# Kernel optimization log

Measured on AMD Instinct MI355X. Metric: run time of the kernel, lower is better.

## Reference

```python
import jax, jax.numpy as jnp
import numpy as np

N, E = 50000, 800000
F_IN, HID, HEADS = 128, 32, 8
H1 = HID * HEADS            # 256: conv1 concat output, also conv2 in/out
NUM_WALKS, WALK_LEN = 512, 64
WINDOW, NEG_S = 5, 10
TEMP = 0.07
NEG_SLOPE = 0.2


def setup_inputs() -> dict:
    key = jax.random.key(0)
    ks = jax.random.split(key, 16)
    inp = {
        "x": jax.random.normal(ks[0], (N, F_IN), jnp.float32),
        "edge_index": jax.random.randint(ks[1], (2, E), 0, N),
        "walks": jax.random.randint(ks[2], (NUM_WALKS, WALK_LEN), 0, N),
        "neg_nodes": jax.random.randint(ks[3], (NUM_WALKS, WALK_LEN, NEG_S), 0, N),
        # conv1 params (GATConv: in=F_IN, out=HID, heads=HEADS, concat)
        "W1": jax.random.normal(ks[4], (F_IN, HEADS * HID), jnp.float32) / np.sqrt(F_IN),
        "a_src1": jax.random.normal(ks[5], (HEADS, HID), jnp.float32) / np.sqrt(HID),
        "a_dst1": jax.random.normal(ks[6], (HEADS, HID), jnp.float32) / np.sqrt(HID),
        "b1": jnp.zeros((HEADS * HID,), jnp.float32),
        # conv2 params (GATConv: in=H1, out=H1, heads=1)
        "W2": jax.random.normal(ks[7], (H1, H1), jnp.float32) / np.sqrt(H1),
        "a_src2": jax.random.normal(ks[8], (1, H1), jnp.float32) / np.sqrt(H1),
        "a_dst2": jax.random.normal(ks[9], (1, H1), jnp.float32) / np.sqrt(H1),
        "b2": jnp.zeros((H1,), jnp.float32),
    }
    return inp


def gat_conv(x, edge_index, W, a_src, a_dst, b, heads, out_ch):
    """PyG-style GATConv: self-loops, per-dst softmax attention, concat heads."""
    n = x.shape[0]
    loops = jnp.arange(n)
    src = jnp.concatenate([edge_index[0], loops])
    dst = jnp.concatenate([edge_index[1], loops])
    xw = (x @ W).reshape(n, heads, out_ch)                  # [N,H,C]
    al_s = jnp.einsum('nhc,hc->nh', xw, a_src)              # [N,H]
    al_d = jnp.einsum('nhc,hc->nh', xw, a_dst)
    e = jax.nn.leaky_relu(al_s[src] + al_d[dst], NEG_SLOPE)  # [Et,H]
    m = jax.ops.segment_max(e, dst, num_segments=n)
    ex = jnp.exp(e - m[dst])
    den = jax.ops.segment_sum(ex, dst, num_segments=n)
    alpha = ex / den[dst]                                    # [Et,H]
    out = jax.ops.segment_sum(alpha[:, :, None] * xw[src], dst, num_segments=n)
    return out.reshape(n, heads * out_ch) + b


def walk_contrastive_loss(emb, walks, neg_nodes):
    eps = 1e-8
    nrm = emb / jnp.clip(jnp.linalg.norm(emb, axis=-1, keepdims=True), eps)
    L = walks.shape[1]
    offs = jnp.concatenate([jnp.arange(-WINDOW, 0), jnp.arange(1, WINDOW + 1)])  # [2W]
    pos_pos = jnp.arange(L)[:, None] + offs[None, :]        # [L,2W]
    pos_valid = (pos_pos >= 0) & (pos_pos < L)
    pos_nodes = walks[:, jnp.clip(pos_pos, 0, L - 1)]       # [B,L,2W]
    anchor = nrm[walks]                                      # [B,L,D]
    pos_sims = jnp.einsum('bld,blpd->blp', anchor, nrm[pos_nodes]) / TEMP
    neg_sims = jnp.einsum('bld,blsd->bls', anchor, nrm[neg_nodes]) / TEMP
    # drop negatives that collide with (valid) positives, as torch.isin filter does
    neg_in_pos = ((neg_nodes[:, :, :, None] == pos_nodes[:, :, None, :])
                  & pos_valid[None, :, None, :]).any(-1)     # [B,L,S]
    pos_sum = jnp.sum(jnp.exp(pos_sims) * pos_valid[None].astype(emb.dtype), axis=-1)
    neg_sum = jnp.sum(jnp.exp(neg_sims) * (~neg_in_pos).astype(emb.dtype), axis=-1)
    has_pos = pos_valid.any(-1)[None]                        # [1,L]
    safe_pos = jnp.where(has_pos, pos_sum, 1.0)
    term = -jnp.log(safe_pos / (safe_pos + neg_sum))
    return jnp.sum(jnp.where(has_pos, term, 0.0))


def reference(x, edge_index, walks, neg_nodes, W1, a_src1, a_dst1, b1,
              W2, a_src2, a_dst2, b2):
    emb1 = jax.nn.elu(gat_conv(x, edge_index, W1, a_src1, a_dst1, b1, HEADS, HID))
    emb2 = gat_conv(emb1, edge_index, W2, a_src2, a_dst2, b2, 1, H1)
    emb = jnp.concatenate([emb1, emb2], axis=1)              # [N, 2*H1]
    return walk_contrastive_loss(emb, walks, neg_nodes)
```

## Files before the change

### kernel.cpp

```cpp
#include <hip/hip_runtime.h>
#include <math.h>

#define N_NODES 50000
#define N_PAD 50048
#define E_EDGES 800000
#define E_PAD (E_EDGES + 8 * N_NODES)
#define FDIM_IN 128
#define HID_1 32
#define HEADS_1 8
#define H1DIM 256
#define NUM_WALKS 512
#define WALK_LEN 64
#define WINDOW 5
#define NEG_S 10
#define TEMP 0.07f
#define INV_TEMP (1.0f / 0.07f)
#define NEG_SLOPE 0.2f
#define LOG2E 1.44269504f

#define SCAN_BLOCKS ((N_NODES + 255) / 256)

typedef unsigned int uint;
typedef unsigned short ushort;
typedef long long i64_t;
typedef __attribute__((ext_vector_type(8))) short bf16x8;
typedef __attribute__((ext_vector_type(8))) ushort us8;
typedef __attribute__((ext_vector_type(4))) float f32x4;
typedef __attribute__((ext_vector_type(2))) float vf2;

__device__ __forceinline__ float leaky(float v) {
    return fmaxf(v, v * NEG_SLOPE);
}

__device__ __forceinline__ float bfl(uint u) { return __uint_as_float(u << 16); }
__device__ __forceinline__ float bfh(uint u) { return __uint_as_float(u & 0xffff0000u); }

__device__ __forceinline__ ushort f2bf(float x) {
    uint u = __float_as_uint(x);
    u = u + 0x7fffu + ((u >> 16) & 1u);
    return (ushort)(u >> 16);
}

__device__ __forceinline__ uint pk4fp8(float a, float b, float c, float d) {
    int u = __builtin_amdgcn_cvt_pk_fp8_f32(a, b, 0, false);
    u = __builtin_amdgcn_cvt_pk_fp8_f32(c, d, u, true);
    return (uint)u;
}


#define PB_CVT  6250
#define PB_DEG  3125
#define PB_FILL ((E_PAD / 2 + 255) / 256)
#define PO_DEG  (PB_CVT)
#define PO_FILL (PO_DEG + PB_DEG)
#define PO_WT1  (PO_FILL + PB_FILL)
#define PO_WT2  (PO_WT1 + 128)
#define PO_MISC (PO_WT2 + 256)
#define PREP_GRID (PO_MISC + 1)

__global__ __launch_bounds__(256) void prep_kernel(
        const float* __restrict__ x, const int* __restrict__ ei,
        const float* __restrict__ W1, const float* __restrict__ W2,
        uint* __restrict__ xb, ushort* __restrict__ wt1, ushort* __restrict__ wt2,
        int* __restrict__ deg, uint* __restrict__ srl_u,
        float* __restrict__ als1, float* __restrict__ als2, uint* __restrict__ xw8) {
    const int blk = blockIdx.x, t = threadIdx.x;
    if (blk < PB_CVT) {
        int i = blk * 256 + t;
        float4 v = ((const float4*)x)[i];
        uint2 p;
        p.x = (uint)f2bf(v.x) | ((uint)f2bf(v.y) << 16);
        p.y = (uint)f2bf(v.z) | ((uint)f2bf(v.w) << 16);
        ((uint2*)xb)[i] = p;
    } else if (blk < PO_FILL) {
        int e = (blk - PO_DEG) * 256 + t;
        atomicAdd(&deg[ei[E_EDGES + e]], 1);
    } else if (blk < PO_WT1) {
        int i = (blk - PO_FILL) * 256 + t;
        if (i < E_PAD / 2) srl_u[i] = 0xC350C350u;
    } else if (blk < PO_WT2) {
        int tid = (blk - PO_WT1) * 256 + t;
        int k = tid >> 8, n = tid & 255;
        wt1[n * 128 + k] = f2bf(W1[k * 256 + n]);
    } else if (blk < PO_MISC) {
        int tid = (blk - PO_WT2) * 256 + t;
        int k = tid >> 8, n = tid & 255;
        wt2[n * 256 + k] = f2bf(W2[k * 256 + n]);
    } else {
        if (t < HEADS_1) als1[N_NODES * HEADS_1 + t] = -1e30f;
        if (t == HEADS_1) als2[N_NODES] = -1e30f;
        if (t >= 64 && t < 128) xw8[N_NODES * 64 + (t - 64)] = 0u;
    }
}


__global__ __launch_bounds__(256) void scan_a(const int* __restrict__ deg,
                                              int* __restrict__ excl,
                                              int* __restrict__ bsum) {
    __shared__ int s[256];
    int t = threadIdx.x;
    int i = blockIdx.x * 256 + t;
    int d = (i < N_NODES) ? deg[i] : 0;
    int v = (d + 7) & ~7;
    s[t] = v;
    __syncthreads();
    for (int off = 1; off < 256; off <<= 1) {
        int tmp = (t >= off) ? s[t - off] : 0;
        __syncthreads();
        s[t] += tmp;
        __syncthreads();
    }
    if (i < N_NODES) excl[i] = s[t] - v;
    if (t == 255) bsum[blockIdx.x] = s[255];
}

__global__ __launch_bounds__(256) void scan_b(int* __restrict__ bsum) {
    __shared__ int s[256];
    int t = threadIdx.x;
    int v = (t < SCAN_BLOCKS) ? bsum[t] : 0;
    s[t] = v;
    __syncthreads();
    for (int off = 1; off < 256; off <<= 1) {
        int tmp = (t >= off) ? s[t - off] : 0;
        __syncthreads();
        s[t] += tmp;
        __syncthreads();
    }
    if (t < SCAN_BLOCKS) bsum[t] = s[t] - v;
}

__global__ void scan_c2(const int* __restrict__ deg,
                        int* __restrict__ excl, const int* __restrict__ bsum,
                        int* __restrict__ row_start) {
    int i = blockIdx.x * blockDim.x + threadIdx.x;
    if (i < N_NODES) {
        int rs = excl[i] + bsum[i >> 8];
        row_start[i] = rs;
        if (i == N_NODES - 1) row_start[N_NODES] = rs + ((deg[i] + 7) & ~7);
    }
}

__global__ void bucket_kernel(const int* __restrict__ ei,
                              const int* __restrict__ row_start,
                              int* __restrict__ cursor,
                              ushort* __restrict__ srclist) {
    int e = blockIdx.x * blockDim.x + threadIdx.x;
    if (e >= E_EDGES) return;
    int dst = ei[E_EDGES + e];
    int pos = atomicAdd(&cursor[dst], 1);
    srclist[row_start[dst] + pos] = (ushort)ei[e];
}

template<int K, int H>
__global__ __launch_bounds__(256) void mfma_gemm64(
        const ushort* __restrict__ A,
        const ushort* __restrict__ Wt,
        uint* __restrict__ Y8,
        const float* __restrict__ a_src,
        const float* __restrict__ a_dst,
        float* __restrict__ als, float* __restrict__ ald) {
    constexpr int KP = K + 8;
    constexpr int K8 = K / 8;
    __shared__ __align__(16) ushort As[64 * KP];
    __shared__ float sals[64][5], sald[64][5];
    const int m0 = blockIdx.x * 64;
    const int t = threadIdx.x;
    const uint4* Ag = (const uint4*)(A + (size_t)m0 * K);
    uint4* As4 = (uint4*)As;
    for (int i = t; i < 64 * K8; i += 256) {
        int r = i / K8, c8 = i % K8;
        As4[r * (K8 + 1) + c8] = Ag[i];
    }
    __syncthreads();
    const int wv = __builtin_amdgcn_readfirstlane(t >> 6);
    const int lane = t & 63;
    const int n0 = wv * 64;
    const int mrow = lane & 15, q = lane >> 4;
    f32x4 acc[4][4];
#pragma unroll
    for (int mt = 0; mt < 4; mt++)
#pragma unroll
        for (int i = 0; i < 4; i++) acc[mt][i] = (f32x4){0.f, 0.f, 0.f, 0.f};
#pragma unroll
    for (int k0 = 0; k0 < K; k0 += 32) {
        bf16x8 a[4], b[4];
#pragma unroll
        for (int mt = 0; mt < 4; mt++)
            a[mt] = *(const bf16x8*)(As + (mt * 16 + mrow) * KP + k0 + q * 8);
#pragma unroll
        for (int i = 0; i < 4; i++)
            b[i] = *(const bf16x8*)(Wt + (uint)(n0 + i * 16 + mrow) * K + k0 + q * 8);
#pragma unroll
        for (int mt = 0; mt < 4; mt++)
#pragma unroll
            for (int i = 0; i < 4; i++)
                acc[mt][i] = __builtin_amdgcn_mfma_f32_16x16x32_bf16(a[mt], b[i], acc[mt][i], 0, 0, 0);
    }
    {
        float as[4], ad[4];
#pragma unroll
        for (int i = 0; i < 4; i++) {
            as[i] = a_src[n0 + i * 16 + mrow];
            ad[i] = a_dst[n0 + i * 16 + mrow];
        }
#pragma unroll
        for (int mt = 0; mt < 4; mt++) {
#pragma unroll
            for (int r = 0; r < 4; r++) {
                const int row = m0 + mt * 16 + q * 4 + r;
                if (H == 8) {
                    float ps0 = acc[mt][0][r] * as[0] + acc[mt][1][r] * as[1];
                    float ps1 = acc[mt][2][r] * as[2] + acc[mt][3][r] * as[3];
                    float pd0 = acc[mt][0][r] * ad[0] + acc[mt][1][r] * ad[1];
                    float pd1 = acc[mt][2][r] * ad[2] + acc[mt][3][r] * ad[3];
#pragma unroll
                    for (int o = 1; o < 16; o <<= 1) {
                        ps0 += __shfl_xor(ps0, o, 64); ps1 += __shfl_xor(ps1, o, 64);
                        pd0 += __shfl_xor(pd0, o, 64); pd1 += __shfl_xor(pd1, o, 64);
                    }
                    if (mrow == 0 && row < N_NODES) {
                        als[row * 8 + 2 * wv] = ps0 * LOG2E;
                        als[row * 8 + 2 * wv + 1] = ps1 * LOG2E;
                        ald[row * 8 + 2 * wv] = pd0 * LOG2E;
                        ald[row * 8 + 2 * wv + 1] = pd1 * LOG2E;
                    }
                } else {
                    float ps = acc[mt][0][r] * as[0] + acc[mt][1][r] * as[1]
                             + acc[mt][2][r] * as[2] + acc[mt][3][r] * as[3];
                    float pd = acc[mt][0][r] * ad[0] + acc[mt][1][r] * ad[1]
                             + acc[mt][2][r] * ad[2] + acc[mt][3][r] * ad[3];
#pragma unroll
                    for (int o = 1; o < 16; o <<= 1) {
                        ps += __shfl_xor(ps, o, 64); pd += __shfl_xor(pd, o, 64);
                    }
                    if (mrow == 0) {
                        sals[mt * 16 + q * 4 + r][wv] = ps;
                        sald[mt * 16 + q * 4 + r][wv] = pd;
                    }
                }
            }
        }
    }
    __syncthreads();
    if (H == 1 && t < 64) {
        const int row = m0 + t;
        if (row < N_NODES) {
            als[row] = (sals[t][0] + sals[t][1] + sals[t][2] + sals[t][3]) * LOG2E;
            ald[row] = (sald[t][0] + sald[t][1] + sald[t][2] + sald[t][3]) * LOG2E;
        }
    }
    float* S = (float*)As + wv * 16 * 68;
    const int prow = lane >> 2, pj = lane & 3;
#pragma unroll
    for (int mt = 0; mt < 4; mt++) {
#pragma unroll
        for (int i = 0; i < 4; i++)
#pragma unroll
            for (int r = 0; r < 4; r++)
                S[(q * 4 + r) * 68 + i * 16 + mrow] = acc[mt][i][r];
        const float* cp = S + prow * 68 + pj * 16;
        uint4 o;
        o.x = pk4fp8(cp[0],  cp[1],  cp[2],  cp[3]);
        o.y = pk4fp8(cp[4],  cp[5],  cp[6],  cp[7]);
        o.z = pk4fp8(cp[8],  cp[9],  cp[10], cp[11]);
        o.w = pk4fp8(cp[12], cp[13], cp[14], cp[15]);
        const int row = m0 + mt * 16 + prow;
        if (row < N_NODES)
            ((uint4*)(Y8 + (size_t)row * 64))[wv * 4 + pj] = o;
    }
}

__global__ __launch_bounds__(256) void gat_gather1(
        const int* __restrict__ row_start, const ushort* __restrict__ srclist,
        const float* __restrict__ als, const float* __restrict__ ald,
        const uint* __restrict__ xw8,
        const float* __restrict__ bias,
        ushort* __restrict__ emb1b) {
    const int wid = __builtin_amdgcn_readfirstlane(blockIdx.x * 4 + (threadIdx.x >> 6));
    const uint lane = threadIdx.x & 63;
    const uint h = lane >> 3;
    const float ald_n = ald[wid * HEADS_1 + h];
    const int beg = row_start[wid], end = row_start[wid + 1];

    float ex0 = __builtin_amdgcn_exp2f(leaky(als[wid * HEADS_1 + h] + ald_n));
    uint u = xw8[((uint)wid << 6) + lane];
    vf2 lo = __builtin_amdgcn_cvt_pk_f32_fp8((int)u, false);
    vf2 hi = __builtin_amdgcn_cvt_pk_f32_fp8((int)u, true);
    float den = ex0;
    vf2 exv0 = {ex0, ex0};
    vf2 a01 = exv0 * lo, a23 = exv0 * hi;

    for (int i = beg; i < end; i += 8) {
        us8 sv = *(const us8*)(srclist + i);
        uint rr[8]; float ee[8];
#pragma unroll
        for (int j = 0; j < 8; j++) rr[j] = xw8[((uint)sv[j] << 6) + lane];
#pragma unroll
        for (int j = 0; j < 8; j++) ee[j] = als[(uint)sv[j] * HEADS_1 + h];
#pragma unroll
        for (int j = 0; j < 8; j++) {
            float ex = __builtin_amdgcn_exp2f(leaky(ee[j] + ald_n));
            vf2 l2 = __builtin_amdgcn_cvt_pk_f32_fp8((int)rr[j], false);
            vf2 h2 = __builtin_amdgcn_cvt_pk_f32_fp8((int)rr[j], true);
            den += ex;
            vf2 exv = {ex, ex};
            a01 += exv * l2;
            a23 += exv * h2;
        }
    }
    float inv = 1.f / den;
    float4 bv = ((const float4*)bias)[lane];
    float4 r;
    r.x = a01[0] * inv + bv.x; r.y = a01[1] * inv + bv.y;
    r.z = a23[0] * inv + bv.z; r.w = a23[1] * inv + bv.w;
    r.x = r.x > 0.f ? r.x : __expf(r.x) - 1.f;
    r.y = r.y > 0.f ? r.y : __expf(r.y) - 1.f;
    r.z = r.z > 0.f ? r.z : __expf(r.z) - 1.f;
    r.w = r.w > 0.f ? r.w : __expf(r.w) - 1.f;
    uint2 p;
    p.x = (uint)f2bf(r.x) | ((uint)f2bf(r.y) << 16);
    p.y = (uint)f2bf(r.z) | ((uint)f2bf(r.w) << 16);
    ((uint2*)emb1b)[((uint)wid << 6) + lane] = p;
}

__global__ __launch_bounds__(256) void gat_gather2(
        const int* __restrict__ row_start, const ushort* __restrict__ srclist,
        const float* __restrict__ als, const float* __restrict__ ald,
        const uint* __restrict__ xw8,
        const float* __restrict__ bias,
        const ushort* __restrict__ emb1b,
        uint* __restrict__ embn8) {
    const int wid = __builtin_amdgcn_readfirstlane(blockIdx.x * 4 + (threadIdx.x >> 6));
    const uint lane = threadIdx.x & 63;
    const float ald_n = ald[wid];
    const int beg = row_start[wid], end = row_start[wid + 1];

    float ex0 = __builtin_amdgcn_exp2f(leaky(als[wid] + ald_n));
    uint u = xw8[((uint)wid << 6) + lane];
    vf2 lo = __builtin_amdgcn_cvt_pk_f32_fp8((int)u, false);
    vf2 hi = __builtin_amdgcn_cvt_pk_f32_fp8((int)u, true);
    float den = ex0;
    vf2 exv0 = {ex0, ex0};
    vf2 a01 = exv0 * lo, a23 = exv0 * hi;

    for (int i = beg; i < end; i += 8) {
        us8 sv = *(const us8*)(srclist + i);
        uint rr[8]; float ee[8];
#pragma unroll
        for (int j = 0; j < 8; j++) rr[j] = xw8[((uint)sv[j] << 6) + lane];
#pragma unroll
        for (int j = 0; j < 8; j++) ee[j] = als[(uint)sv[j]];
#pragma unroll
        for (int j = 0; j < 8; j++) {
            float ex = __builtin_amdgcn_exp2f(leaky(ee[j] + ald_n));
            vf2 l2 = __builtin_amdgcn_cvt_pk_f32_fp8((int)rr[j], false);
            vf2 h2 = __builtin_amdgcn_cvt_pk_f32_fp8((int)rr[j], true);
            den += ex;
            vf2 exv = {ex, ex};
            a01 += exv * l2;
            a23 += exv * h2;
        }
    }
    float inv = 1.f / den;
    float4 bv = ((const float4*)bias)[lane];
    float4 e2;
    e2.x = a01[0] * inv + bv.x; e2.y = a01[1] * inv + bv.y;
    e2.z = a23[0] * inv + bv.z; e2.w = a23[1] * inv + bv.w;
    uint2 u1 = ((const uint2*)emb1b)[((uint)wid << 6) + lane];
    float4 e1;
    e1.x = bfl(u1.x); e1.y = bfh(u1.x); e1.z = bfl(u1.y); e1.w = bfh(u1.y);

    float ssum = e1.x * e1.x + e1.y * e1.y + e1.z * e1.z + e1.w * e1.w
               + e2.x * e2.x + e2.y * e2.y + e2.z * e2.z + e2.w * e2.w;
#pragma unroll
    for (int o = 32; o > 0; o >>= 1) ssum += __shfl_xor(ssum, o, 64);
    float innv = 1.f / fmaxf(sqrtf(ssum), 1e-8f);

    uint p1 = pk4fp8(e1.x * innv, e1.y * innv, e1.z * innv, e1.w * innv);
    uint p2 = pk4fp8(e2.x * innv, e2.y * innv, e2.z * innv, e2.w * innv);
    embn8[((uint)wid << 7) + lane] = p1;
    embn8[((uint)wid << 7) + 64 + lane] = p2;
}


#define ROWU 130

__global__ __launch_bounds__(1024, 8) void loss_mfma_kernel(
        const uint* __restrict__ embn8,
        const int* __restrict__ walks, const int* __restrict__ negs,
        float* __restrict__ out) {
    __shared__ __align__(16) uint srows8[WALK_LEN * ROWU];
    __shared__ int wids[WALK_LEN];
    __shared__ int snid[WALK_LEN * NEG_S];
    __shared__ float possum[WALK_LEN];
    __shared__ float negsum[WALK_LEN];
    const int b = blockIdx.x;
    const int t = threadIdx.x;
    const int w = __builtin_amdgcn_readfirstlane(t >> 6);
    const int lane = t & 63;
    if (t < 64) wids[t] = walks[b * WALK_LEN + t];
    else if (t < 704) snid[t - 64] = negs[b * WALK_LEN * NEG_S + (t - 64)];
    else if (t < 768) possum[t - 704] = 0.f;
    else if (t < 832) negsum[t - 768] = 0.f;
    __syncthreads();
    for (int r = w; r < WALK_LEN; r += 16)
        ((uint2*)(srows8 + r * ROWU))[lane] = ((const uint2*)(embn8 + ((uint)wids[r] << 7)))[lane];
    __syncthreads();

    const int mrow = lane & 15, q = lane >> 4;
    const char* embc = (const char*)embn8;

    for (int job = w; job < 48; job += 16) {
        f32x4 acc0 = {0.f, 0.f, 0.f, 0.f};
        f32x4 acc1 = {0.f, 0.f, 0.f, 0.f};
        if (job < 40) {
            const int g = job / 10;
            const int albase = g * 16;
            const char* ap = (const char*)(srows8 + (albase + mrow) * ROWU) + q * 8;
            const int c = job * 16 + mrow;
            const int node = snid[c];
            const char* bp = embc + (((uint)node << 9) + (uint)(q * 8));
#pragma unroll
            for (int k0 = 0; k0 < 256; k0 += 32) {
                i64_t a0 = *(const i64_t*)(ap + k0);
                i64_t b0 = *(const i64_t*)(bp + k0);
                acc0 = __builtin_amdgcn_mfma_f32_16x16x32_fp8_fp8(a0, b0, acc0, 0, 0, 0);
                i64_t a1 = *(const i64_t*)(ap + k0 + 256);
                i64_t b1 = *(const i64_t*)(bp + k0 + 256);
                acc1 = __builtin_amdgcn_mfma_f32_16x16x32_fp8_fp8(a1, b1, acc1, 0, 0, 0);
            }
            const int owner = c / 10;
#pragma unroll
            for (int reg = 0; reg < 4; reg++) {
                const int l_a = albase + q * 4 + reg;
                float e = 0.f;
                if (owner == l_a) {
                    bool msk = false;
#pragma unroll
                    for (int dj = -WINDOW; dj <= WINDOW; dj++) {
                        if (dj == 0) continue;
                        int p = l_a + dj;
                        if (p >= 0 && p < WALK_LEN && wids[p] == node) msk = true;
                    }
                    if (!msk) e = __expf((acc0[reg] + acc1[reg]) * INV_TEMP);
                }
#pragma unroll
                for (int o = 1; o < 16; o <<= 1) e += __shfl_xor(e, o, 64);
                if (mrow == 0 && e != 0.f) atomicAdd(&negsum[l_a], e);
            }
        } else {
            const int pj = job - 40;
            const int g = pj >> 1, half = pj & 1;
            const int albase = g * 16;
            const int base = (albase - WINDOW) > 0 ? (albase - WINDOW) : 0;
            const int hi = (albase + 15 + WINDOW) < (WALK_LEN - 1) ? (albase + 15 + WINDOW) : (WALK_LEN - 1);
            const int cnt = hi - base + 1;
            const char* ap = (const char*)(srows8 + (albase + mrow) * ROWU) + q * 8;
            const int r = half * 16 + mrow;
            const int row = base + r;
            const int rc = row < hi ? row : hi;
            const char* bp = (const char*)(srows8 + rc * ROWU) + q * 8;
#pragma unroll
            for (int k0 = 0; k0 < 256; k0 += 32) {
                i64_t a0 = *(const i64_t*)(ap + k0);
                i64_t b0 = *(const i64_t*)(bp + k0);
                acc0 = __builtin_amdgcn_mfma_f32_16x16x32_fp8_fp8(a0, b0, acc0, 0, 0, 0);
                i64_t a1 = *(const i64_t*)(ap + k0 + 256);
                i64_t b1 = *(const i64_t*)(bp + k0 + 256);
                acc1 = __builtin_amdgcn_mfma_f32_16x16x32_fp8_fp8(a1, b1, acc1, 0, 0, 0);
            }
#pragma unroll
            for (int reg = 0; reg < 4; reg++) {
                const int l_a = albase + q * 4 + reg;
                const int d = row - l_a;
                bool use = (r < cnt) && (d != 0) && (d >= -WINDOW) && (d <= WINDOW);
                float e = use ? __expf((acc0[reg] + acc1[reg]) * INV_TEMP) : 0.f;
#pragma unroll
                for (int o = 1; o < 16; o <<= 1) e += __shfl_xor(e, o, 64);
                if (mrow == 0 && e != 0.f) atomicAdd(&possum[l_a], e);
            }
        }
    }
    __syncthreads();
    if (t < 64) {
        float term = logf(1.f + negsum[t] / possum[t]);
#pragma unroll
        for (int o = 32; o > 0; o >>= 1) term += __shfl_xor(term, o, 64);
        if (t == 0) atomicAdd(out, term);
    }
}

extern "C" void kernel_launch(void* const* d_in, const int* in_sizes, int n_in,
                              void* d_out, int out_size, void* d_ws, size_t ws_size,
                              hipStream_t stream) {
    const float* x      = (const float*)d_in[0];
    const int*   ei     = (const int*)d_in[1];
    const int*   walks  = (const int*)d_in[2];
    const int*   negs   = (const int*)d_in[3];
    const float* W1     = (const float*)d_in[4];
    const float* a_src1 = (const float*)d_in[5];
    const float* a_dst1 = (const float*)d_in[6];
    const float* b1     = (const float*)d_in[7];
    const float* W2     = (const float*)d_in[8];
    const float* a_src2 = (const float*)d_in[9];
    const float* a_dst2 = (const float*)d_in[10];
    const float* b2     = (const float*)d_in[11];
    float* out = (float*)d_out;

    float* ws = (float*)d_ws;
    size_t off = 0;
#define ALIGN_OFF off = (off + 255) & ~(size_t)255
    float* r_xw8   = ws + off; off += (size_t)(N_NODES + 1) * 64;  ALIGN_OFF;
    float* r_emb1b = ws + off; off += (size_t)N_PAD * 128;         ALIGN_OFF;
    float* r_embn8 = ws + off; off += (size_t)N_NODES * 128;       ALIGN_OFF;
    float* r_xb    = ws + off; off += (size_t)N_PAD * 64;          ALIGN_OFF;
    float* r_wt1   = ws + off; off += 256 * 64;                    ALIGN_OFF;
    float* r_wt2   = ws + off; off += 256 * 128;                   ALIGN_OFF;
    float* als1  = ws + off; off += (N_NODES + 1) * HEADS_1;       ALIGN_OFF;
    float* ald1  = ws + off; off += N_NODES * HEADS_1;             ALIGN_OFF;
    float* als2  = ws + off; off += N_NODES + 1;                   ALIGN_OFF;
    float* ald2  = ws + off; off += N_NODES;                       ALIGN_OFF;
    int* deg       = (int*)(ws + off); off += N_NODES;             ALIGN_OFF;
    int* excl      = (int*)(ws + off); off += N_NODES;             ALIGN_OFF;
    int* bsum      = (int*)(ws + off); off += 256;                 ALIGN_OFF;
    int* row_start = (int*)(ws + off); off += N_NODES + 1;         ALIGN_OFF;
    int* cursor    = (int*)(ws + off); off += N_NODES;             ALIGN_OFF;
    ushort* srclist = (ushort*)(ws + off); off += E_PAD / 2;       ALIGN_OFF;
    uint*   xw8   = (uint*)r_xw8;
    ushort* emb1b = (ushort*)r_emb1b;
    uint*   embn8 = (uint*)r_embn8;
    ushort* xb    = (ushort*)r_xb;
    ushort* wt1   = (ushort*)r_wt1;
    ushort* wt2   = (ushort*)r_wt2;

    hipMemsetAsync(out, 0, sizeof(float) * out_size, stream);
    hipMemsetAsync(deg, 0, sizeof(int) * N_NODES, stream);
    hipMemsetAsync(cursor, 0, sizeof(int) * N_NODES, stream);

    prep_kernel<<<PREP_GRID, 256, 0, stream>>>(
        x, ei, W1, W2, (uint*)xb, wt1, wt2, deg, (uint*)srclist, als1, als2, xw8);

    scan_a<<<SCAN_BLOCKS, 256, 0, stream>>>(deg, excl, bsum);
    scan_b<<<1, 256, 0, stream>>>(bsum);
    scan_c2<<<SCAN_BLOCKS, 256, 0, stream>>>(deg, excl, bsum, row_start);
    bucket_kernel<<<(E_EDGES + 255) / 256, 256, 0, stream>>>(ei, row_start, cursor, srclist);

    mfma_gemm64<128, HEADS_1><<<N_PAD / 64, 256, 0, stream>>>(
        xb, wt1, xw8, a_src1, a_dst1, als1, ald1);
    gat_gather1<<<N_NODES / 4, 256, 0, stream>>>(
        row_start, srclist, als1, ald1, xw8, b1, emb1b);

    mfma_gemm64<256, 1><<<N_PAD / 64, 256, 0, stream>>>(
        emb1b, wt2, xw8, a_src2, a_dst2, als2, ald2);
    gat_gather2<<<N_NODES / 4, 256, 0, stream>>>(
        row_start, srclist, als2, ald2, xw8, b2, emb1b, embn8);

    loss_mfma_kernel<<<NUM_WALKS, 1024, 0, stream>>>(embn8, walks, negs, out);
}
```

Baseline: 351.6 us.

## Prefetch negative rows into registers and permute fp8 layout for 16-byte loads

The normalizer now writes fp8 embeddings in a permuted k-order, so each MFMA lane can fetch two consecutive k-chunks with one 16-byte load instead of two 8-byte loads. The loss kernel drops the shared negative-index staging: each wave loads its negative node's row straight into registers, overlapping that with the shared-row fill, and prefetches the next job's row while the current MFMAs run. The 16-lane reductions use DPP instead of shuffles, and the shared row pitch changes to fit 16-byte accesses. This costs more registers per thread (eight uint4 buffers) and relies on the permuted layout matching the MFMA k-split in both operands.

```diff
diff --git a/kernel.cpp b/kernel.cpp
--- a/kernel.cpp
+++ b/kernel.cpp
@@ -27,6 +27,7 @@
 typedef __attribute__((ext_vector_type(8))) ushort us8;
 typedef __attribute__((ext_vector_type(4))) float f32x4;
 typedef __attribute__((ext_vector_type(2))) float vf2;
+typedef __attribute__((ext_vector_type(2))) i64_t i64x2;
 
 __device__ __forceinline__ float leaky(float v) {
     return fmaxf(v, v * NEG_SLOPE);
@@ -45,6 +46,18 @@
     int u = __builtin_amdgcn_cvt_pk_fp8_f32(a, b, 0, false);
     u = __builtin_amdgcn_cvt_pk_fp8_f32(c, d, u, true);
     return (uint)u;
+}
+
+__device__ __forceinline__ float red16(float x) {
+    int v = __float_as_int(x);
+    x += __int_as_float(__builtin_amdgcn_update_dpp(0, v, 0xB1, 0xF, 0xF, true));
+    v = __float_as_int(x);
+    x += __int_as_float(__builtin_amdgcn_update_dpp(0, v, 0x4E, 0xF, 0xF, true));
+    v = __float_as_int(x);
+    x += __int_as_float(__builtin_amdgcn_update_dpp(0, v, 0x141, 0xF, 0xF, true));
+    v = __float_as_int(x);
+    x += __int_as_float(__builtin_amdgcn_update_dpp(0, v, 0x140, 0xF, 0xF, true));
+    return x;
 }
 
 
@@ -378,12 +391,13 @@
 
     uint p1 = pk4fp8(e1.x * innv, e1.y * innv, e1.z * innv, e1.w * innv);
     uint p2 = pk4fp8(e2.x * innv, e2.y * innv, e2.z * innv, e2.w * innv);
-    embn8[((uint)wid << 7) + lane] = p1;
-    embn8[((uint)wid << 7) + 64 + lane] = p2;
-}
-
-
-#define ROWU 130
+    const uint n1 = ((lane >> 4) << 4) | (((lane >> 1) & 3) << 2) | (((lane >> 3) & 1) << 1) | (lane & 1);
+    embn8[((uint)wid << 7) + n1] = p1;
+    embn8[((uint)wid << 7) + 64 + n1] = p2;
+}
+
+
+#define ROWU 140
 
 __global__ __launch_bounds__(1024, 8) void loss_mfma_kernel(
         const uint* __restrict__ embn8,
@@ -391,45 +405,68 @@
         float* __restrict__ out) {
     __shared__ __align__(16) uint srows8[WALK_LEN * ROWU];
     __shared__ int wids[WALK_LEN];
-    __shared__ int snid[WALK_LEN * NEG_S];
     __shared__ float possum[WALK_LEN];
     __shared__ float negsum[WALK_LEN];
     const int b = blockIdx.x;
     const int t = threadIdx.x;
     const int w = __builtin_amdgcn_readfirstlane(t >> 6);
     const int lane = t & 63;
-    if (t < 64) wids[t] = walks[b * WALK_LEN + t];
-    else if (t < 704) snid[t - 64] = negs[b * WALK_LEN * NEG_S + (t - 64)];
-    else if (t < 768) possum[t - 704] = 0.f;
-    else if (t < 832) negsum[t - 768] = 0.f;
-    __syncthreads();
-    for (int r = w; r < WALK_LEN; r += 16)
-        ((uint2*)(srows8 + r * ROWU))[lane] = ((const uint2*)(embn8 + ((uint)wids[r] << 7)))[lane];
-    __syncthreads();
-
     const int mrow = lane & 15, q = lane >> 4;
     const char* embc = (const char*)embn8;
 
-    for (int job = w; job < 48; job += 16) {
+    if (t < 64) wids[t] = walks[b * WALK_LEN + t];
+    else if (t < 128) possum[t - 64] = 0.f;
+    else if (t < 192) negsum[t - 128] = 0.f;
+
+    uint4 Bv[8];
+    int pnode = negs[b * (WALK_LEN * NEG_S) + (w * 16 + mrow)];
+    {
+        const char* bp = embc + (((uint)pnode) << 9) + (uint)(q * 16);
+#pragma unroll
+        for (int j = 0; j < 8; j++) Bv[j] = *(const uint4*)(bp + j * 64);
+    }
+    __syncthreads();
+
+    {
+        const int rA = w * 4 + (lane >> 5);
+        const int rB = rA + 2;
+        const uint off = lane & 31;
+        ((uint4*)(srows8 + rA * ROWU))[off] = ((const uint4*)embn8)[((uint)wids[rA] << 5) + off];
+        ((uint4*)(srows8 + rB * ROWU))[off] = ((const uint4*)embn8)[((uint)wids[rB] << 5) + off];
+    }
+    __syncthreads();
+
+#pragma unroll
+    for (int ji = 0; ji < 3; ji++) {
+        const int job = w + ji * 16;
         f32x4 acc0 = {0.f, 0.f, 0.f, 0.f};
         f32x4 acc1 = {0.f, 0.f, 0.f, 0.f};
-        if (job < 40) {
-            const int g = job / 10;
-            const int albase = g * 16;
-            const char* ap = (const char*)(srows8 + (albase + mrow) * ROWU) + q * 8;
-            const int c = job * 16 + mrow;
-            const int node = snid[c];
-            const char* bp = embc + (((uint)node << 9) + (uint)(q * 8));
-#pragma unroll
-            for (int k0 = 0; k0 < 256; k0 += 32) {
-                i64_t a0 = *(const i64_t*)(ap + k0);
-                i64_t b0 = *(const i64_t*)(bp + k0);
-                acc0 = __builtin_amdgcn_mfma_f32_16x16x32_fp8_fp8(a0, b0, acc0, 0, 0, 0);
-                i64_t a1 = *(const i64_t*)(ap + k0 + 256);
-                i64_t b1 = *(const i64_t*)(bp + k0 + 256);
-                acc1 = __builtin_amdgcn_mfma_f32_16x16x32_fp8_fp8(a1, b1, acc1, 0, 0, 0);
-            }
-            const int owner = c / 10;
+        if (ji < 2 || w < 8) {
+            const int albase = (job / 10) * 16;
+            const int curnode = pnode;
+            const int owner = (job * 16 + mrow) / 10;
+            const char* ap = (const char*)(srows8 + (albase + mrow) * ROWU) + q * 16;
+#pragma unroll
+            for (int j = 0; j < 4; j++) {
+                i64x2 a = *(const i64x2*)(ap + j * 64);
+                const i64x2 bb = *(const i64x2*)&Bv[j];
+                acc0 = __builtin_amdgcn_mfma_f32_16x16x32_fp8_fp8(a[0], bb[0], acc0, 0, 0, 0);
+                acc0 = __builtin_amdgcn_mfma_f32_16x16x32_fp8_fp8(a[1], bb[1], acc0, 0, 0, 0);
+            }
+#pragma unroll
+            for (int j = 4; j < 8; j++) {
+                i64x2 a = *(const i64x2*)(ap + j * 64);
+                const i64x2 bb = *(const i64x2*)&Bv[j];
+                acc1 = __builtin_amdgcn_mfma_f32_16x16x32_fp8_fp8(a[0], bb[0], acc1, 0, 0, 0);
+                acc1 = __builtin_amdgcn_mfma_f32_16x16x32_fp8_fp8(a[1], bb[1], acc1, 0, 0, 0);
+            }
+            if (ji == 0 || (ji == 1 && w < 8)) {
+                const int njob = job + 16;
+                pnode = negs[b * (WALK_LEN * NEG_S) + (njob * 16 + mrow)];
+                const char* bp = embc + (((uint)pnode) << 9) + (uint)(q * 16);
+#pragma unroll
+                for (int j = 0; j < 8; j++) Bv[j] = *(const uint4*)(bp + j * 64);
+            }
 #pragma unroll
             for (int reg = 0; reg < 4; reg++) {
                 const int l_a = albase + q * 4 + reg;
@@ -440,34 +477,38 @@
                     for (int dj = -WINDOW; dj <= WINDOW; dj++) {
                         if (dj == 0) continue;
                         int p = l_a + dj;
-                        if (p >= 0 && p < WALK_LEN && wids[p] == node) msk = true;
+                        if (p >= 0 && p < WALK_LEN && wids[p] == curnode) msk = true;
                     }
                     if (!msk) e = __expf((acc0[reg] + acc1[reg]) * INV_TEMP);
                 }
-#pragma unroll
-                for (int o = 1; o < 16; o <<= 1) e += __shfl_xor(e, o, 64);
+                e = red16(e);
                 if (mrow == 0 && e != 0.f) atomicAdd(&negsum[l_a], e);
             }
         } else {
-            const int pj = job - 40;
+            const int pj = w - 8;
             const int g = pj >> 1, half = pj & 1;
             const int albase = g * 16;
             const int base = (albase - WINDOW) > 0 ? (albase - WINDOW) : 0;
             const int hi = (albase + 15 + WINDOW) < (WALK_LEN - 1) ? (albase + 15 + WINDOW) : (WALK_LEN - 1);
             const int cnt = hi - base + 1;
-            const char* ap = (const char*)(srows8 + (albase + mrow) * ROWU) + q * 8;
             const int r = half * 16 + mrow;
             const int row = base + r;
             const int rc = row < hi ? row : hi;
-            const char* bp = (const char*)(srows8 + rc * ROWU) + q * 8;
-#pragma unroll
-            for (int k0 = 0; k0 < 256; k0 += 32) {
-                i64_t a0 = *(const i64_t*)(ap + k0);
-                i64_t b0 = *(const i64_t*)(bp + k0);
-                acc0 = __builtin_amdgcn_mfma_f32_16x16x32_fp8_fp8(a0, b0, acc0, 0, 0, 0);
-                i64_t a1 = *(const i64_t*)(ap + k0 + 256);
-                i64_t b1 = *(const i64_t*)(bp + k0 + 256);
-                acc1 = __builtin_amdgcn_mfma_f32_16x16x32_fp8_fp8(a1, b1, acc1, 0, 0, 0);
+            const char* ap = (const char*)(srows8 + (albase + mrow) * ROWU) + q * 16;
+            const char* bp = (const char*)(srows8 + rc * ROWU) + q * 16;
+#pragma unroll
+            for (int j = 0; j < 4; j++) {
+                i64x2 a = *(const i64x2*)(ap + j * 64);
+                i64x2 bb = *(const i64x2*)(bp + j * 64);
+                acc0 = __builtin_amdgcn_mfma_f32_16x16x32_fp8_fp8(a[0], bb[0], acc0, 0, 0, 0);
+                acc0 = __builtin_amdgcn_mfma_f32_16x16x32_fp8_fp8(a[1], bb[1], acc0, 0, 0, 0);
+            }
+#pragma unroll
+            for (int j = 4; j < 8; j++) {
+                i64x2 a = *(const i64x2*)(ap + j * 64);
+                i64x2 bb = *(const i64x2*)(bp + j * 64);
+                acc1 = __builtin_amdgcn_mfma_f32_16x16x32_fp8_fp8(a[0], bb[0], acc1, 0, 0, 0);
+                acc1 = __builtin_amdgcn_mfma_f32_16x16x32_fp8_fp8(a[1], bb[1], acc1, 0, 0, 0);
             }
 #pragma unroll
             for (int reg = 0; reg < 4; reg++) {
@@ -475,8 +516,7 @@
                 const int d = row - l_a;
                 bool use = (r < cnt) && (d != 0) && (d >= -WINDOW) && (d <= WINDOW);
                 float e = use ? __expf((acc0[reg] + acc1[reg]) * INV_TEMP) : 0.f;
-#pragma unroll
-                for (int o = 1; o < 16; o <<= 1) e += __shfl_xor(e, o, 64);
+                e = red16(e);
                 if (mrow == 0 && e != 0.f) atomicAdd(&possum[l_a], e);
             }
         }
```

Result: no change. 346.8 us (-1.4%).
